# Performance work log

Hardware: AMD Instinct MI355X
Metric: run time of the kernel (lower is better)

Reference implementation:

```python
import jax, jax.numpy as jnp
import numpy as np

B, CH, H, W, D = 2, 32, 256, 512, 192


def setup_inputs() -> dict:
    key = jax.random.key(0)
    ks = jax.random.split(key, 10)
    def w(k, shape, fan_in):
        return jax.random.normal(k, shape, jnp.float32) * (1.0 / np.sqrt(fan_in))
    return {
        "x": jax.random.normal(ks[0], (B, CH, H, W), jnp.float32),
        "y": jax.random.normal(ks[1], (B, CH, H, W), jnp.float32),
        # encoder: 1x1 convs ch->64->32->1 (shared for x and y)
        "w1": w(ks[2], (64, CH), CH), "b1": w(ks[3], (64,), CH),
        "w2": w(ks[4], (32, 64), 64), "b2": w(ks[5], (32,), 64),
        "w3": w(ks[6], (1, 32), 32), "b3": w(ks[7], (1,), 32),
        # decoderl: 1x1 conv maxdisp->maxdisp (original code applies decoderl to BOTH volumes)
        "wd": w(ks[8], (D, D), D), "bd": w(ks[9], (D,), D),
    }


def _conv1x1(w, b, h):  # [O,C] x [B,C,H,W] -> [B,O,H,W]
    return jnp.einsum("oc,bchw->bohw", w, h) + b[None, :, None, None]


def _encoder(x, w1, b1, w2, b2, w3, b3):
    h = jax.nn.relu(x)
    h = jax.nn.relu(_conv1x1(w1, b1, h))
    h = jax.nn.relu(_conv1x1(w2, b2, h))
    h = jax.nn.relu(_conv1x1(w3, b3, h))
    return h[:, 0]  # squeeze channel -> [B,H,W]


def _cost_volumes(xf, yf):
    # costx[b,d,h,w] = xf[b,h,w+d] * yf[b,h,w]   (0 where w+d >= W)
    # costy[b,d,h,w] = xf[b,h,w]   * yf[b,h,w-d] (0 where w-d < 0)
    dgrid = jnp.arange(D)
    wgrid = jnp.arange(W)
    x_pad = jnp.pad(xf, ((0, 0), (0, 0), (0, D)))          # zero pad right
    xg = x_pad[:, :, wgrid[None, :] + dgrid[:, None]]       # [B,H,D,W]
    costx = (xg * yf[:, :, None, :]).transpose(0, 2, 1, 3)  # [B,D,H,W]
    y_pad = jnp.pad(yf, ((0, 0), (0, 0), (D, 0)))           # zero pad left
    yg = y_pad[:, :, wgrid[None, :] - dgrid[:, None] + D]   # [B,H,D,W]
    costy = (xf[:, :, None, :] * yg).transpose(0, 2, 1, 3)  # [B,D,H,W]
    return costx, costy


def reference(x, y, w1, b1, w2, b2, w3, b3, wd, bd):
    xf = _encoder(x, w1, b1, w2, b2, w3, b3)
    yf = _encoder(y, w1, b1, w2, b2, w3, b3)
    costx, costy = _cost_volumes(xf, yf)
    probx = jax.nn.softmax(_conv1x1(wd, bd, costx), axis=1)
    proby = jax.nn.softmax(_conv1x1(wd, bd, costy), axis=1)  # decoderl used for both, as in source
    disp_vals = jnp.arange(D, dtype=probx.dtype)
    dispx = jnp.einsum("bdhw,d->bhw", probx, disp_vals)
    dispy = jnp.einsum("bdhw,d->bhw", proby, disp_vals)
    return dispx, dispy
```

## Files before the change

### kernel.cpp

```cpp
#include <hip/hip_runtime.h>


typedef __attribute__((ext_vector_type(8)))  __bf16 bf16x8;
typedef __attribute__((ext_vector_type(4)))  float  f32x4;
typedef __attribute__((ext_vector_type(16))) float  f32x16;

#define MFMA32(a,b,c) __builtin_amdgcn_mfma_f32_32x32x16_bf16((a),(b),(c),0,0,0)
#define MFMA16(a,b,c) __builtin_amdgcn_mfma_f32_16x16x32_bf16((a),(b),(c),0,0,0)

constexpr int WW  = 512;
constexpr int HW  = 256 * 512;
constexpr int CHW = 32 * HW;
constexpr float LOG2E = 1.4426950408889634f;

constexpr size_t XFB_OFF = 0;
constexpr int    STB     = 25600;
constexpr size_t WDP_OFF = 2 * 262144 * 2;
constexpr size_t BDP_OFF = WDP_OFF + 3 * STB;

__global__ __launch_bounds__(512)
void panet_encode(const float* __restrict__ gx,  const float* __restrict__ gy,
                  const float* __restrict__ gw1, const float* __restrict__ gb1,
                  const float* __restrict__ gw2, const float* __restrict__ gb2,
                  const float* __restrict__ gw3, const float* __restrict__ gb3,
                  const float* __restrict__ gwd, const float* __restrict__ gbd,
                  char* __restrict__ ws)
{
  const int blk = blockIdx.x;
  const int tid = threadIdx.x;

  if (blk >= 1024) {
    const int pi = blk - 1024;
    unsigned short* wdp = (unsigned short*)(ws + WDP_OFF);
    for (int idx = tid; idx < 12 * 200; idx += 512) {
      const int oo = idx / 200;
      const int k  = idx - oo * 200;
      const int o  = 12 * pi + oo;
      unsigned short v = 0;
      if (k < 192) v = __builtin_bit_cast(unsigned short, (__bf16)gwd[o * 192 + k]);
      wdp[(o >> 6) * 12800 + (o & 63) * 200 + k] = v;
    }
    if (pi == 0) {
      float* bdp = (float*)(ws + BDP_OFF);
      if (tid < 192) bdp[tid] = gbd[tid] * LOG2E;
    }
    return;
  }

  const int t    = blk >> 9;
  const int bh   = blk & 511;
  const int lane = tid & 63;
  const int m    = lane & 15;
  const int g    = lane >> 4;
  const int wid  = tid >> 6;

  bf16x8 A1[4], A2[2][2];
  f32x4  bias1[4], bias2[2], w3v[2];
  #pragma unroll
  for (int Mt = 0; Mt < 4; ++Mt) {
    const float* p = gw1 + (16 * Mt + m) * 32 + 4 * g;
    const f32x4 u0 = *(const f32x4*)p;
    const f32x4 u1 = *(const f32x4*)(p + 16);
    #pragma unroll
    for (int j = 0; j < 4; ++j) { A1[Mt][j] = (__bf16)u0[j]; A1[Mt][j + 4] = (__bf16)u1[j]; }
    bias1[Mt] = *(const f32x4*)(gb1 + 16 * Mt + 4 * g);
  }
  #pragma unroll
  for (int Mt = 0; Mt < 2; ++Mt) {
    #pragma unroll
    for (int s = 0; s < 2; ++s) {
      const float* p = gw2 + (16 * Mt + m) * 64 + 32 * s + 4 * g;
      const f32x4 u0 = *(const f32x4*)p;
      const f32x4 u1 = *(const f32x4*)(p + 16);
      #pragma unroll
      for (int j = 0; j < 4; ++j) { A2[Mt][s][j] = (__bf16)u0[j]; A2[Mt][s][j + 4] = (__bf16)u1[j]; }
    }
    bias2[Mt] = *(const f32x4*)(gb2 + 16 * Mt + 4 * g);
    w3v[Mt]   = *(const f32x4*)(gw3 + 16 * Mt + 4 * g);
  }
  const float b3s = gb3[0];
  const f32x4 zf4 = {0.f, 0.f, 0.f, 0.f};
  const float* base = (t ? gy : gx) + (bh >> 8) * CHW + (bh & 255) * WW;
  unsigned short* xfb = (unsigned short*)(ws + XFB_OFF) + t * 262144 + bh * 512;

  for (int u = wid; u < 32; u += 8) {
    const int w0 = u << 4;
    const float* src = base + w0 + m;

    bf16x8 B1;
    #pragma unroll
    for (int j = 0; j < 8; ++j) {
      const int c = 16 * (j >> 2) + 4 * g + (j & 3);
      B1[j] = (__bf16)fmaxf(src[c * HW], 0.f);
    }
    f32x4 acc1[4];
    #pragma unroll
    for (int Mt = 0; Mt < 4; ++Mt) acc1[Mt] = MFMA16(A1[Mt], B1, zf4);

    bf16x8 B2[2];
    #pragma unroll
    for (int s = 0; s < 2; ++s) {
      #pragma unroll
      for (int j = 0; j < 4; ++j) {
        B2[s][j]     = (__bf16)fmaxf(acc1[2 * s][j]     + bias1[2 * s][j],     0.f);
        B2[s][j + 4] = (__bf16)fmaxf(acc1[2 * s + 1][j] + bias1[2 * s + 1][j], 0.f);
      }
    }
    f32x4 acc2[2];
    #pragma unroll
    for (int Mt = 0; Mt < 2; ++Mt)
      acc2[Mt] = MFMA16(A2[Mt][1], B2[1], MFMA16(A2[Mt][0], B2[0], zf4));

    float s3 = 0.f;
    #pragma unroll
    for (int Mt = 0; Mt < 2; ++Mt)
      #pragma unroll
      for (int r = 0; r < 4; ++r)
        s3 += w3v[Mt][r] * fmaxf(acc2[Mt][r] + bias2[Mt][r], 0.f);
    s3 += __shfl_xor(s3, 16);
    s3 += __shfl_xor(s3, 32);
    const float val = fmaxf(s3 + b3s, 0.f);

    if (lane < 16)
      xfb[w0 + m] = __builtin_bit_cast(unsigned short, (__bf16)val);
  }
}

constexpr int CPS    = 1424;
constexpr int K2_HK  = 76800;
constexpr int K2_BD  = K2_HK + 8 * CPS;
constexpr int K2_LDS = K2_BD + 768;

__global__ __launch_bounds__(512)
void panet_corr(const char* __restrict__ ws, float* __restrict__ gout)
{
  extern __shared__ __align__(16) char lds[];
  const int blk  = blockIdx.x;
  const int dir  = blk >> 9;
  const int bh   = blk & 511;
  const int tid  = threadIdx.x;
  const int lane = tid & 63;
  const int l31  = lane & 31;
  const int h    = lane >> 5;
  const int wid  = tid >> 6;

  const unsigned short* xfbu = (const unsigned short*)(ws + XFB_OFF);
  const unsigned short* hs = xfbu + (dir ? 262144 : 0) + bh * 512;
  const unsigned short* ss = xfbu + (dir ? 0 : 262144) + bh * 512;

  {
    const f32x4* src = (const f32x4*)(ws + WDP_OFF);
    f32x4* dst = (f32x4*)lds;
    #pragma unroll 5
    for (int i = tid; i < 4800; i += 512) dst[i] = src[i];
    if (tid < 192)
      ((float*)(lds + K2_BD))[tid] = ((const float*)(ws + BDP_OFF))[tid];
  }
  for (int e = tid; e < 712; e += 512) {
    #pragma unroll
    for (int c = 0; c < 8; ++c) {
      const int j = e + c;
      unsigned short v = 0;
      if (j <= 511) v = hs[dir ? (511 - j) : j];
      ((unsigned short*)(lds + K2_HK + c * CPS))[e] = v;
    }
  }
  __syncthreads();

  const char* bptr[2]; float sc[2];
  #pragma unroll
  for (int ct = 0; ct < 2; ++ct) {
    const int col = wid * 64 + ct * 32 + l31;
    const int I0  = dir ? (511 - col) : col;
    const int cc  = I0 & 7;
    bptr[ct] = lds + K2_HK + cc * CPS + 2 * (I0 - cc) + 16 * h;
    sc[ct]  = LOG2E * __builtin_bit_cast(float, (unsigned)ss[col] << 16);
  }

  float stS0 = 0.f, stS1 = 0.f, stW0 = 0.f, stW1 = 0.f;

  int s = wid % 3;
  for (int si = 0; si < 3; ++si) {
    const char* abase = lds + (64 * s + l31) * 400 + 16 * h;
    f32x16 a00 = {0}, a01 = {0}, a10 = {0}, a11 = {0};
    #pragma unroll 2
    for (int ks = 0; ks < 12; ++ks) {
      const bf16x8 af0 = *(const bf16x8*)(abase + 32 * ks);
      const bf16x8 af1 = *(const bf16x8*)(abase + 12800 + 32 * ks);
      const bf16x8 bf0 = *(const bf16x8*)(bptr[0] + 32 * ks);
      const bf16x8 bf1 = *(const bf16x8*)(bptr[1] + 32 * ks);
      a00 = MFMA32(af0, bf0, a00);
      a01 = MFMA32(af0, bf1, a01);
      a10 = MFMA32(af1, bf0, a10);
      a11 = MFMA32(af1, bf1, a11);
    }

    const float obase = (float)(64 * s + 4 * h);
    #pragma unroll
    for (int ct = 0; ct < 2; ++ct) {
      float ls0 = 0.f, ls1 = 0.f, lw0 = 0.f, lw1 = 0.f;
      #pragma unroll
      for (int q = 0; q < 4; ++q) {
        const f32x4 bd0 = *(const f32x4*)(lds + K2_BD + (64 * s + 8 * q + 4 * h) * 4);
        const f32x4 bd1 = *(const f32x4*)(lds + K2_BD + (64 * s + 8 * q + 4 * h + 32) * 4);
        #pragma unroll
        for (int r = 0; r < 4; ++r) {
          const int i = 4 * q + r;
          const float L0 = fmaf(sc[ct], (ct ? a01 : a00)[i], bd0[r]);
          const float L1 = fmaf(sc[ct], (ct ? a11 : a10)[i], bd1[r]);
          const float p0 = __builtin_amdgcn_exp2f(L0);
          const float p1 = __builtin_amdgcn_exp2f(L1);
          const float c  = (float)(r + 8 * q);
          ls0 += p0;  ls1 += p1;
          lw0 = fmaf(c, p0, lw0);
          lw1 = fmaf(c + 32.f, p1, lw1);
        }
      }
      const float ls = ls0 + ls1;
      const float lw = fmaf(obase, ls, lw0 + lw1);
      if (ct == 0) { stS0 += ls; stW0 += lw; }
      else         { stS1 += ls; stW1 += lw; }
    }

    s = (s == 2) ? 0 : (s + 1);
  }

  float* outp = gout + dir * 262144 + bh * 512;
  #pragma unroll
  for (int ct = 0; ct < 2; ++ct) {
    float sr = ct ? stS1 : stS0;
    float wr = ct ? stW1 : stW0;
    sr += __shfl_xor(sr, 32);
    wr += __shfl_xor(wr, 32);
    if (lane < 32) outp[wid * 64 + ct * 32 + l31] = wr / sr;
  }
}

extern "C" void kernel_launch(void* const* d_in, const int* in_sizes, int n_in,
                              void* d_out, int out_size, void* d_ws, size_t ws_size,
                              hipStream_t stream) {
  const float* x  = (const float*)d_in[0];
  const float* y  = (const float*)d_in[1];
  const float* w1 = (const float*)d_in[2];
  const float* b1 = (const float*)d_in[3];
  const float* w2 = (const float*)d_in[4];
  const float* b2 = (const float*)d_in[5];
  const float* w3 = (const float*)d_in[6];
  const float* b3 = (const float*)d_in[7];
  const float* wd = (const float*)d_in[8];
  const float* bd = (const float*)d_in[9];
  char* ws = (char*)d_ws;

  (void)hipFuncSetAttribute((const void*)panet_corr,
                            hipFuncAttributeMaxDynamicSharedMemorySize, K2_LDS);
  panet_encode<<<1040, 512, 0, stream>>>(x, y, w1, b1, w2, b2, w3, b3, wd, bd, ws);
  panet_corr<<<1024, 512, K2_LDS, stream>>>(ws, (float*)d_out);
}
```

Measured before the change: 84.58 us.

## Split corr blocks in half, stream weight stripes through LDS, keep B fragments in registers

The correlation kernel now launches 2048 blocks of 256 threads, each handling half a row. Instead of holding all three decoder-weight stripes in LDS, it keeps one stripe at a time and reloads it between disparity stripes with extra barriers. The cost-row B fragments are preloaded into registers once and reused across all stripes. This cuts LDS use per block from about 89KB to about 37KB so more blocks can be resident, at the cost of reloading the weights per block, serialized barriers and higher register pressure.

New measurement: 167.0 us. 97.5% more time.

```diff
diff --git a/kernel.cpp b/kernel.cpp
--- a/kernel.cpp
+++ b/kernel.cpp
@@ -127,17 +127,19 @@
 }
 
 constexpr int CPS    = 1424;
-constexpr int K2_HK  = 76800;
-constexpr int K2_BD  = K2_HK + 8 * CPS;
+constexpr int K2_WD  = 0;
+constexpr int K2_HK  = STB;
+constexpr int K2_BD  = K2_HK + 11392;
 constexpr int K2_LDS = K2_BD + 768;
 
-__global__ __launch_bounds__(512)
+__global__ __launch_bounds__(256)
 void panet_corr(const char* __restrict__ ws, float* __restrict__ gout)
 {
-  extern __shared__ __align__(16) char lds[];
+  __shared__ __align__(16) char lds[K2_LDS];
   const int blk  = blockIdx.x;
-  const int dir  = blk >> 9;
-  const int bh   = blk & 511;
+  const int dir  = blk >> 10;
+  const int bh   = (blk >> 1) & 511;
+  const int ch2  = blk & 1;
   const int tid  = threadIdx.x;
   const int lane = tid & 63;
   const int l31  = lane & 31;
@@ -150,13 +152,13 @@
 
   {
     const f32x4* src = (const f32x4*)(ws + WDP_OFF);
-    f32x4* dst = (f32x4*)lds;
-    #pragma unroll 5
-    for (int i = tid; i < 4800; i += 512) dst[i] = src[i];
+    f32x4* dst = (f32x4*)(lds + K2_WD);
+    #pragma unroll 2
+    for (int i = tid; i < 1600; i += 256) dst[i] = src[i];
     if (tid < 192)
       ((float*)(lds + K2_BD))[tid] = ((const float*)(ws + BDP_OFF))[tid];
   }
-  for (int e = tid; e < 712; e += 512) {
+  for (int e = tid; e < 712; e += 256) {
     #pragma unroll
     for (int c = 0; c < 8; ++c) {
       const int j = e + c;
@@ -167,32 +169,45 @@
   }
   __syncthreads();
 
-  const char* bptr[2]; float sc[2];
+  int boff[2]; float sc[2];
   #pragma unroll
   for (int ct = 0; ct < 2; ++ct) {
-    const int col = wid * 64 + ct * 32 + l31;
+    const int col = ch2 * 256 + wid * 64 + ct * 32 + l31;
     const int I0  = dir ? (511 - col) : col;
     const int cc  = I0 & 7;
-    bptr[ct] = lds + K2_HK + cc * CPS + 2 * (I0 - cc) + 16 * h;
+    boff[ct] = K2_HK + cc * CPS + 2 * (I0 - cc) + 16 * h;
     sc[ct]  = LOG2E * __builtin_bit_cast(float, (unsigned)ss[col] << 16);
   }
 
+  bf16x8 bfr[12][2];
+  #pragma unroll
+  for (int ks = 0; ks < 12; ++ks) {
+    bfr[ks][0] = *(const bf16x8*)(lds + boff[0] + 32 * ks);
+    bfr[ks][1] = *(const bf16x8*)(lds + boff[1] + 32 * ks);
+  }
+
   float stS0 = 0.f, stS1 = 0.f, stW0 = 0.f, stW1 = 0.f;
 
-  int s = wid % 3;
-  for (int si = 0; si < 3; ++si) {
-    const char* abase = lds + (64 * s + l31) * 400 + 16 * h;
+  for (int s = 0; s < 3; ++s) {
+    if (s) {
+      __syncthreads();
+      const f32x4* src = (const f32x4*)(ws + WDP_OFF + s * STB);
+      f32x4* dst = (f32x4*)(lds + K2_WD);
+      #pragma unroll 2
+      for (int i = tid; i < 1600; i += 256) dst[i] = src[i];
+    }
+    __syncthreads();
+
+    const char* abase = lds + K2_WD + l31 * 400 + 16 * h;
     f32x16 a00 = {0}, a01 = {0}, a10 = {0}, a11 = {0};
     #pragma unroll 2
     for (int ks = 0; ks < 12; ++ks) {
       const bf16x8 af0 = *(const bf16x8*)(abase + 32 * ks);
       const bf16x8 af1 = *(const bf16x8*)(abase + 12800 + 32 * ks);
-      const bf16x8 bf0 = *(const bf16x8*)(bptr[0] + 32 * ks);
-      const bf16x8 bf1 = *(const bf16x8*)(bptr[1] + 32 * ks);
-      a00 = MFMA32(af0, bf0, a00);
-      a01 = MFMA32(af0, bf1, a01);
-      a10 = MFMA32(af1, bf0, a10);
-      a11 = MFMA32(af1, bf1, a11);
+      a00 = MFMA32(af0, bfr[ks][0], a00);
+      a01 = MFMA32(af0, bfr[ks][1], a01);
+      a10 = MFMA32(af1, bfr[ks][0], a10);
+      a11 = MFMA32(af1, bfr[ks][1], a11);
     }
 
     const float obase = (float)(64 * s + 4 * h);
@@ -221,11 +236,9 @@
       if (ct == 0) { stS0 += ls; stW0 += lw; }
       else         { stS1 += ls; stW1 += lw; }
     }
-
-    s = (s == 2) ? 0 : (s + 1);
-  }
-
-  float* outp = gout + dir * 262144 + bh * 512;
+  }
+
+  float* outp = gout + dir * 262144 + bh * 512 + ch2 * 256;
   #pragma unroll
   for (int ct = 0; ct < 2; ++ct) {
     float sr = ct ? stS1 : stS0;
@@ -251,8 +264,6 @@
   const float* bd = (const float*)d_in[9];
   char* ws = (char*)d_ws;
 
-  (void)hipFuncSetAttribute((const void*)panet_corr,
-                            hipFuncAttributeMaxDynamicSharedMemorySize, K2_LDS);
   panet_encode<<<1040, 512, 0, stream>>>(x, y, w1, b1, w2, b2, w3, b3, wd, bd, ws);
-  panet_corr<<<1024, 512, K2_LDS, stream>>>(ws, (float*)d_out);
+  panet_corr<<<2048, 256, 0, stream>>>(ws, (float*)d_out);
 }
```
